# Kernel optimization log

Measured on AMD Instinct MI355X. Metric: run time of the kernel, lower is better.

## Reference

```python
import jax, jax.numpy as jnp
import numpy as np

HDIM = 1024
CDIM = 256
TEMPER = 10.0
IGNORE_OUT = 0.0
EPS = 1e-6


def setup_inputs() -> dict:
    key = jax.random.key(0)
    ks = jax.random.split(key, 6)
    B, T, D = 2, 128, 384
    x = jax.random.normal(ks[0], (B, T, D), jnp.float32)
    y = jax.random.normal(ks[1], (B, T, D), jnp.float32)
    # xavier-normal style init for the two linear layers
    W_enc = jax.random.normal(ks[2], (D, HDIM), jnp.float32) * np.sqrt(2.0 / (D + HDIM))
    b_enc = jnp.zeros((HDIM,), jnp.float32)
    W_dec = jax.random.normal(ks[3], (HDIM, D), jnp.float32) * np.sqrt(2.0 / (D + HDIM))
    b_dec = jnp.zeros((D,), jnp.float32)
    return {"x": x, "y": y, "W_enc": W_enc, "b_enc": b_enc, "W_dec": W_dec, "b_dec": b_dec}


def reference(x, y, W_enc, b_enc, W_dec, b_dec):
    B, T, D = x.shape
    n_iter = HDIM // CDIM
    pad = D - 1
    # shift_idx[s, j] = s + j : window of width D at offset s, s in [0, 2D-2]
    shift_idx = jnp.arange(2 * D - 1)[:, None] + jnp.arange(D)[None, :]

    seq_mask = (y == IGNORE_OUT)                       # (B,T,D) bool
    denom_seq = jnp.sum(~seq_mask).astype(x.dtype)
    qn = jnp.linalg.norm(y, axis=-1)                   # (B,T)

    mask_prev = None
    x_dis, losses = [], []
    for _ in range(n_iter):
        # --- _pad_for_shift: (B,T,2D-1,D) shifted windows of x ---
        kp = jnp.pad(x, ((0, 0), (0, 0), (pad, pad)))  # (B,T,3D-2)
        kpt = kp[..., shift_idx]                       # (B,T,2D-1,D)
        # --- _score (cos) + argmax over shifts ---
        kn = jnp.linalg.norm(kpt, axis=-1)             # (B,T,2D-1)
        sim = jnp.einsum('btsd,btd->bts', kpt, y) / (qn[..., None] * kn + EPS)
        sim = jnp.where(jnp.isnan(sim), 0.0, sim)
        theta = jnp.argmax(sim, axis=-1)               # (B,T) int
        x_opt = jnp.take_along_axis(kpt, theta[..., None, None], axis=-2)[..., 0, :]  # (B,T,D)
        # --- attention: elementwise cos-scaled score, temp softmax, detached ---
        dn = (jnp.linalg.norm(x_opt, axis=-1, keepdims=True)
              * jnp.linalg.norm(y, axis=-1, keepdims=True) + EPS)
        attn = jax.nn.softmax((x_opt * y / dn) / TEMPER, axis=-1)
        attn = jnp.where(jnp.isnan(attn), 0.0, attn)
        attn = jax.lax.stop_gradient(attn)
        x_attn = x_opt * attn
        # --- _reverse_pad_for_shift: window at offset 2D-2-theta ---
        kp2 = jnp.pad(x_attn, ((0, 0), (0, 0), (pad, pad)))
        rev_idx = (2 * D - 2 - theta)[..., None] + jnp.arange(D)  # (B,T,D)
        x_ele = jnp.take_along_axis(kp2, rev_idx, axis=-1)         # (B,T,D)
        # --- self_net: encoder -> top-k sparsify -> decoder_self ---
        h = x_ele @ W_enc + b_enc                      # (B,T,HDIM)
        if mask_prev is not None:
            h = jnp.where(mask_prev > 0, 1e-10, h)
        _, idx_top = jax.lax.top_k(h, CDIM)            # (B,T,CDIM)
        flat = idx_top.reshape(B * T, CDIM)
        mask_cur = jnp.zeros((B * T, HDIM), x.dtype).at[
            jnp.arange(B * T)[:, None], flat].set(1.0).reshape(B, T, HDIM)
        if mask_prev is None:
            mask_prev = mask_cur
        else:
            mask_prev = mask_prev + mask_cur - mask_prev * mask_cur
        h = h * mask_cur
        out = h @ W_dec + b_dec                        # (B,T,D)
        x_dis.append(out)
        # --- SeqLoss (masked MSE, mean-reduced by count of valid elems) ---
        err = jnp.where(seq_mask, 0.0, (out - x) ** 2) / denom_seq
        losses.append(jnp.sum(err))
    return jnp.stack(x_dis), jnp.stack(losses)
```

## Files before the change

### kernel.cpp

```cpp
#include <hip/hip_runtime.h>
#include <hip/hip_fp16.h>
#include <math.h>

#define DD 384
#define HD 1024
#define CD 256
#define NS 765
#define NITER 4
#define NROWS 256
#define TEMPER_F 10.0f
#define EPSF 1e-6f
#define CUTF 1e-10f

typedef unsigned long long u64;
typedef unsigned int u32;
typedef _Float16 hh2 __attribute__((ext_vector_type(2)));

__device__ __forceinline__ u32 flipf(float f) {
    u32 u = __float_as_uint(f);
    return u ^ ((u32)((int)u >> 31) | 0x80000000u);
}
__device__ __forceinline__ u32 packh2(float a, float b) {
    __half2 p = __floats2half2_rn(a, b);
    return __builtin_bit_cast(u32, p);
}
__device__ __forceinline__ float dot2(u32 a, u32 b, float c) {
#if __has_builtin(__builtin_amdgcn_fdot2)
    return __builtin_amdgcn_fdot2(__builtin_bit_cast(hh2, a),
                                  __builtin_bit_cast(hh2, b), c, false);
#else
    __half2 ah = __builtin_bit_cast(__half2, a);
    __half2 bh = __builtin_bit_cast(__half2, b);
    return fmaf(__half2float(ah.y), __half2float(bh.y),
           fmaf(__half2float(ah.x), __half2float(bh.x), c));
#endif
}

__global__ __launch_bounds__(256) void convert_kernel(
    const float* __restrict__ We, const float* __restrict__ Wd,
    uint4* __restrict__ wencp4, uint2* __restrict__ wd16)
{
    const int t = blockIdx.x * 256 + threadIdx.x;
    if (t < 192 * 256) {
        const int j2 = t >> 8, c4 = t & 255;
        float4 a = *(const float4*)&We[(2 * j2)     * HD + 4 * c4];
        float4 b = *(const float4*)&We[(2 * j2 + 1) * HD + 4 * c4];
        wencp4[j2 * 256 + c4] = make_uint4(packh2(a.x, b.x), packh2(a.y, b.y),
                                           packh2(a.z, b.z), packh2(a.w, b.w));
    }
    for (int i = t; i < (HD * DD) / 4; i += 65536) {
        float4 v = ((const float4*)Wd)[i];
        wd16[i] = make_uint2(packh2(v.x, v.y), packh2(v.z, v.w));
    }
}

__global__ __launch_bounds__(1024) void fused_kernel(
    const float* __restrict__ x, const float* __restrict__ y,
    const u32* __restrict__ wencp, const float* __restrict__ benc,
    const u32* __restrict__ wdec16, const float* __restrict__ bdec,
    float* __restrict__ out_xdis, float* __restrict__ lossp,
    int* __restrict__ ycnt)
{
    const int row  = blockIdx.x;
    const int tid  = threadIdx.x;
    const int lane = tid & 63;
    const int wid  = tid >> 6;

    __shared__ __align__(16) float xpad[1152];
    __shared__ __align__(16) float yr[DD];
    __shared__ u32   xep[192];
    __shared__ __align__(16) float part[4][HD];
    __shared__ __align__(16) u32   hist2[4096];
    __shared__ float spart[4 * 192 * 5];
    __shared__ __align__(16) uint2 dec2[HD];
    __shared__ __align__(16) float4 dpart[8][96];
    __shared__ float wred[16];
    __shared__ int   wredi[16];
    __shared__ float wredn[16];
    __shared__ int   wbase16[16];
    __shared__ float s_sc[4];
    __shared__ int   s_theta;
    __shared__ u32   s_b[3];
    __shared__ int   sbinB[3], srankB[3], s_cc[3];
    __shared__ u32   cand[3][64];
    __shared__ int   wcls[128];
    __shared__ int   sbase[128];
    __shared__ int   cnt8[8];
    __shared__ float loss4[NITER];

    const float* xrow = x + row * DD;
    const float* yrow = y + row * DD;

    for (int i = tid; i < 1152; i += 1024)
        xpad[i] = (i >= DD - 1 && i < 2 * DD - 1) ? xrow[i - (DD - 1)] : 0.f;
    if (tid < DD) yr[tid] = yrow[tid];
    __syncthreads();

    if (tid < 768) {
        const int qid = tid / 192, t = tid - qid * 192;
        const int jb = 24 * qid;
        const float4* xp4 = (const float4*)xpad;
        const float4* yp4 = (const float4*)yr;
        float4 A = xp4[t + jb];
        float d0 = 0.f, d1 = 0.f, d2 = 0.f, d3 = 0.f, n0 = 0.f;
#pragma unroll 8
        for (int jc = 0; jc < 24; ++jc) {
            float4 B = xp4[t + jb + jc + 1];
            float4 Y = yp4[jb + jc];
            d0 += A.x * Y.x; d0 += A.y * Y.y; d0 += A.z * Y.z; d0 += A.w * Y.w;
            d1 += A.y * Y.x; d1 += A.z * Y.y; d1 += A.w * Y.z; d1 += B.x * Y.w;
            d2 += A.z * Y.x; d2 += A.w * Y.y; d2 += B.x * Y.z; d2 += B.y * Y.w;
            d3 += A.w * Y.x; d3 += B.x * Y.y; d3 += B.y * Y.z; d3 += B.z * Y.w;
            n0 += A.x * A.x; n0 += A.y * A.y; n0 += A.z * A.z; n0 += A.w * A.w;
            A = B;
        }
        float* sp = &spart[(qid * 192 + t) * 5];
        sp[0] = d0; sp[1] = d1; sp[2] = d2; sp[3] = d3; sp[4] = n0;
    } else {
        const int i = tid - 768;
        if (i < 192) {
            float y0 = yr[2 * i], y1 = yr[2 * i + 1];
            float p = y0 * y0 + y1 * y1;
            int   c = (y0 != 0.f) + (y1 != 0.f);
            for (int o = 32; o; o >>= 1) {
                p += __shfl_xor(p, o, 64);
                c += __shfl_xor(c, o, 64);
            }
            if (lane == 0) { wred[wid] = p; wredi[wid] = c; }
            cand[i >> 6][i & 63] = 0xFFFFFFFFu;
        } else {
            const int j = i - 192;
            if (j < 3) s_cc[j] = 0;
            else if (j < 11) cnt8[j - 3] = 0;
            else if (j < 15) loss4[j - 11] = 0.f;
        }
        for (int h = i; h < 4096; h += 256) hist2[h] = 0u;
    }
    __syncthreads();

    if (tid < 192) {
        const float qn = sqrtf(wred[12] + wred[13] + wred[14]);
        const int b = tid * 5;
        float d0 = spart[b]     + spart[b + 960]     + spart[b + 1920]     + spart[b + 2880];
        float d1 = spart[b + 1] + spart[b + 961]     + spart[b + 1921]     + spart[b + 2881];
        float d2 = spart[b + 2] + spart[b + 962]     + spart[b + 1922]     + spart[b + 2882];
        float d3 = spart[b + 3] + spart[b + 963]     + spart[b + 1923]     + spart[b + 2883];
        float n0 = spart[b + 4] + spart[b + 964]     + spart[b + 1924]     + spart[b + 2884];
        const float x0 = xpad[4 * tid],       x1 = xpad[4 * tid + 1], x2 = xpad[4 * tid + 2];
        const float e0 = xpad[4 * tid + 384], e1 = xpad[4 * tid + 385], e2 = xpad[4 * tid + 386];
        const float n1 = n0 - x0 * x0 + e0 * e0;
        const float n2 = n1 - x1 * x1 + e1 * e1;
        const float n3 = n2 - x2 * x2 + e2 * e2;
        const int s0 = 4 * tid;
        float sim0 = d0 / (qn * sqrtf(n0) + EPSF);
        float sim1 = d1 / (qn * sqrtf(n1) + EPSF);
        float sim2 = d2 / (qn * sqrtf(n2) + EPSF);
        float sim3 = d3 / (qn * sqrtf(n3) + EPSF);
        float bv = sim0; int bs = s0; float bn = n0;
        if (s0 + 1 < NS && sim1 > bv) { bv = sim1; bs = s0 + 1; bn = n1; }
        if (s0 + 2 < NS && sim2 > bv) { bv = sim2; bs = s0 + 2; bn = n2; }
        if (s0 + 3 < NS && sim3 > bv) { bv = sim3; bs = s0 + 3; bn = n3; }
        for (int o = 32; o; o >>= 1) {
            float v2 = __shfl_xor(bv, o, 64);
            int   i2 = __shfl_xor(bs, o, 64);
            float nn2 = __shfl_xor(bn, o, 64);
            if (v2 > bv || (v2 == bv && i2 < bs)) { bv = v2; bs = i2; bn = nn2; }
        }
        if (lane == 0) { wred[wid] = bv; wredi[wid] = bs; wredn[wid] = bn; }
        if (tid == 0) s_sc[0] = qn;
    }
    if (tid == 960) ycnt[row] = wredi[12] + wredi[13] + wredi[14];
    __syncthreads();

    if (tid == 0) {
        float v = wred[0]; int b = wredi[0]; float nn = wredn[0];
        for (int w = 1; w < 3; ++w)
            if (wred[w] > v || (wred[w] == v && wredi[w] < b)) {
                v = wred[w]; b = wredi[w]; nn = wredn[w];
            }
        s_theta = b;
        s_sc[1] = sqrtf(nn) * s_sc[0] + EPSF;
    }
    __syncthreads();
    const int theta = s_theta;
    const float dn = s_sc[1];

    if (tid < DD) {
        float xo = xpad[theta + tid];
        float ez = expf((xo * yr[tid] / dn) / TEMPER_F);
        float p = ez;
        for (int o = 32; o; o >>= 1) p += __shfl_xor(p, o, 64);
        if (lane == 0) wred[wid] = p;
    }
    __syncthreads();

    if (tid < 192) {
        const float S = wred[0] + wred[1] + wred[2] + wred[3] + wred[4] + wred[5];
        const int off = theta - (DD - 1);
        const int sj = 2 * tid - off;
        float a0 = 0.f, a1 = 0.f;
        if (sj >= 0 && sj < DD) {
            float xo = xpad[theta + sj];
            a0 = xo * (expf((xo * yr[sj] / dn) / TEMPER_F) / S);
        }
        if (sj + 1 >= 0 && sj + 1 < DD) {
            float xo = xpad[theta + sj + 1];
            a1 = xo * (expf((xo * yr[sj + 1] / dn) / TEMPER_F) / S);
        }
        xep[tid] = packh2(a0, a1);
    }
    __syncthreads();

    {
        const int ks = tid >> 8;
        const int c4 = tid & 255;
        const uint4* wq = (const uint4*)wencp + (size_t)(ks * 48) * 256 + c4;
        const u32* xb = xep + ks * 48;
        float4 acc = make_float4(0.f, 0.f, 0.f, 0.f);
#pragma unroll 8
        for (int j2 = 0; j2 < 48; ++j2) {
            u32 xv = xb[j2];
            uint4 w = wq[(size_t)j2 * 256];
            acc.x = dot2(xv, w.x, acc.x);
            acc.y = dot2(xv, w.y, acc.y);
            acc.z = dot2(xv, w.z, acc.z);
            acc.w = dot2(xv, w.w, acc.w);
        }
        *(float4*)&part[ks][4 * c4] = acc;
    }
    __syncthreads();

    const float oh = part[0][tid] + part[1][tid] + part[2][tid] + part[3][tid]
                   + benc[tid];
    const u32 okey = ~flipf(oh);
    atomicAdd(&hist2[okey >> 20], 1u);
    __syncthreads();

    {
        const int t4 = tid << 2;
        const u32 l0 = hist2[t4], l1 = hist2[t4 + 1], l2 = hist2[t4 + 2], l3 = hist2[t4 + 3];
        const int s = (int)(l0 + l1 + l2 + l3);
        int inc = s;
        for (int o = 1; o < 64; o <<= 1) {
            int u = __shfl_up(inc, o, 64);
            if (lane >= o) inc += u;
        }
        if (lane == 63) wredi[wid] = inc;
        __syncthreads();
        if (tid == 0) {
            int acc = 0;
            for (int w = 0; w < 16; ++w) { wbase16[w] = acc; acc += wredi[w]; }
        }
        __syncthreads();
        const int c0 = wbase16[wid] + inc - s;
        const int c1 = c0 + (int)l0, c2 = c1 + (int)l1, c3 = c2 + (int)l2;
        const int c4e = c3 + (int)l3;
#pragma unroll
        for (int i = 0; i < 3; ++i) {
            const int R = 255 + (i << 8);
            if (R >= c0 && R < c1)      { sbinB[i] = t4;     srankB[i] = R - c0; }
            else if (R >= c1 && R < c2) { sbinB[i] = t4 + 1; srankB[i] = R - c1; }
            else if (R >= c2 && R < c3) { sbinB[i] = t4 + 2; srankB[i] = R - c2; }
            else if (R >= c3 && R < c4e){ sbinB[i] = t4 + 3; srankB[i] = R - c3; }
        }
        __syncthreads();
        const int myb = (int)(okey >> 20);
#pragma unroll
        for (int i = 0; i < 3; ++i) {
            if (myb == sbinB[i]) {
                int slot = atomicAdd(&s_cc[i], 1);
                if (slot < 64) cand[i][slot] = okey;
            }
        }
        __syncthreads();
        if (wid < 3) {
            u32 v = cand[wid][lane];
            for (int k2 = 2; k2 <= 64; k2 <<= 1) {
                for (int j = k2 >> 1; j > 0; j >>= 1) {
                    u32 p = __shfl_xor(v, j, 64);
                    const bool takeMin = ((lane & j) == 0) == ((lane & k2) == 0);
                    v = takeMin ? (v < p ? v : p) : (v > p ? v : p);
                }
            }
            if (lane == srankB[wid]) s_b[wid] = v;
        }
        __syncthreads();
    }
    const u32 b1 = s_b[0], b2 = s_b[1], b3 = s_b[2];

    {
        const int myk = (okey <= b1) ? 0 : (okey <= b2) ? 1 : (okey <= b3) ? 2 : 3;
        const int cls = 2 * myk + ((oh > CUTF) ? 0 : 1);
        int myprefix = 0;
        const u64 ltmask = (1ull << lane) - 1;
#pragma unroll
        for (int c = 0; c < 8; ++c) {
            u64 m = __ballot(cls == c);
            if (cls == c) myprefix = __popcll(m & ltmask);
            if (lane == 0) {
                wcls[c * 16 + wid] = (int)__popcll(m);
                atomicAdd(&cnt8[c], (int)__popcll(m));
            }
        }
        __syncthreads();
        if (tid < 128) {
            int v = wcls[tid];
            int inc = v;
            for (int o = 1; o < 64; o <<= 1) {
                int t2 = __shfl_up(inc, o, 64);
                if (lane >= o) inc += t2;
            }
            sbase[tid] = inc - v;
        }
        __syncthreads();
        if (tid >= 64 && tid < 128) sbase[tid] += sbase[63] + wcls[63];
        __syncthreads();
        const int slot = sbase[cls * 16 + wid] + myprefix;
        dec2[slot] = make_uint2(__float_as_uint(oh), (u32)tid * 192u);
    }
    __syncthreads();

    {
        const int g8 = tid >> 7;
        const int k  = g8 >> 1;
        const int hf = g8 & 1;
        const int gg = tid & 127;
        const bool active = (gg < 96);
        int n = 0;
        if (active) n = (k == 0) ? CD : cnt8[2 * k];
        int r  = hf * 128;
        int r1 = n < r + 128 ? n : r + 128;
        if (r1 < r) r1 = r;
        float4 acc = make_float4(0.f, 0.f, 0.f, 0.f);
        const u32* wd = wdec16 + 2 * gg;
        const int base = k * CD;
        for (; r + 8 <= r1; r += 8) {
#pragma unroll
            for (int q = 0; q < 8; q += 2) {
                uint4 dv = *(const uint4*)&dec2[base + r + q];
                u32 vp = packh2(__uint_as_float(dv.x), __uint_as_float(dv.z));
                uint2 w0 = *(const uint2*)(wd + dv.y);
                uint2 w1 = *(const uint2*)(wd + dv.w);
                u32 p0 = (w0.x & 0xffffu) | (w1.x << 16);
                u32 p1 = (w0.x >> 16) | (w1.x & 0xffff0000u);
                u32 p2 = (w0.y & 0xffffu) | (w1.y << 16);
                u32 p3 = (w0.y >> 16) | (w1.y & 0xffff0000u);
                acc.x = dot2(vp, p0, acc.x);
                acc.y = dot2(vp, p1, acc.y);
                acc.z = dot2(vp, p2, acc.z);
                acc.w = dot2(vp, p3, acc.w);
            }
        }
        for (; r + 2 <= r1; r += 2) {
            uint4 dv = *(const uint4*)&dec2[base + r];
            u32 vp = packh2(__uint_as_float(dv.x), __uint_as_float(dv.z));
            uint2 w0 = *(const uint2*)(wd + dv.y);
            uint2 w1 = *(const uint2*)(wd + dv.w);
            u32 p0 = (w0.x & 0xffffu) | (w1.x << 16);
            u32 p1 = (w0.x >> 16) | (w1.x & 0xffff0000u);
            u32 p2 = (w0.y & 0xffffu) | (w1.y << 16);
            u32 p3 = (w0.y >> 16) | (w1.y & 0xffff0000u);
            acc.x = dot2(vp, p0, acc.x);
            acc.y = dot2(vp, p1, acc.y);
            acc.z = dot2(vp, p2, acc.z);
            acc.w = dot2(vp, p3, acc.w);
        }
        if (r < r1) {
            uint2 dv = dec2[base + r];
            float v0 = __uint_as_float(dv.x);
            uint2 w0 = *(const uint2*)(wd + dv.y);
            u32 vlo = packh2(v0, 0.f), vhi = packh2(0.f, v0);
            acc.x = dot2(vlo, w0.x, acc.x);
            acc.y = dot2(vhi, w0.x, acc.y);
            acc.z = dot2(vlo, w0.y, acc.z);
            acc.w = dot2(vhi, w0.y, acc.w);
        }
        if (active) dpart[g8][gg] = acc;
    }
    __syncthreads();

    {
        float l = 0.f;
        if (tid < 512) {
            const int k2 = tid >> 7;
            const int q  = tid & 127;
            if (q < 96) {
                float4 a = dpart[2 * k2][q];
                float4 b = dpart[2 * k2 + 1][q];
                float4 bb = *(const float4*)&bdec[4 * q];
                float4 o4;
                o4.x = a.x + b.x + bb.x;
                o4.y = a.y + b.y + bb.y;
                o4.z = a.z + b.z + bb.z;
                o4.w = a.w + b.w + bb.w;
                *(float4*)&out_xdis[((size_t)k2 * NROWS + row) * DD + 4 * q] = o4;
                float4 xv = *(const float4*)&xrow[4 * q];
                float4 yv = *(const float4*)&yr[4 * q];
                float ee;
                ee = o4.x - xv.x; if (yv.x != 0.f) l += ee * ee;
                ee = o4.y - xv.y; if (yv.y != 0.f) l += ee * ee;
                ee = o4.z - xv.z; if (yv.z != 0.f) l += ee * ee;
                ee = o4.w - xv.w; if (yv.w != 0.f) l += ee * ee;
            }
        }
        for (int o = 32; o; o >>= 1) l += __shfl_xor(l, o, 64);
        if (tid < 512 && lane == 0) atomicAdd(&loss4[tid >> 7], l);
    }
    __syncthreads();
    if (tid < NITER) lossp[row * NITER + tid] = loss4[tid];
}

__global__ __launch_bounds__(256) void finalize2(
    const float* __restrict__ lossp, const int* __restrict__ ycnt,
    float* __restrict__ losses)
{
    const int tid = threadIdx.x, lane = tid & 63, w = tid >> 6;
    __shared__ int ctot[4];
    int c = ycnt[tid];
    for (int o = 32; o; o >>= 1) c += __shfl_xor(c, o, 64);
    if (lane == 0) ctot[w] = c;
    __syncthreads();
    const int total = ctot[0] + ctot[1] + ctot[2] + ctot[3];
    float s = lossp[lane * NITER + w] + lossp[(lane + 64) * NITER + w]
            + lossp[(lane + 128) * NITER + w] + lossp[(lane + 192) * NITER + w];
    for (int o = 32; o; o >>= 1) s += __shfl_xor(s, o, 64);
    if (lane == 0) losses[w] = s / (float)total;
}

extern "C" void kernel_launch(void* const* d_in, const int* in_sizes, int n_in,
                              void* d_out, int out_size, void* d_ws, size_t ws_size,
                              hipStream_t stream) {
    const float* x    = (const float*)d_in[0];
    const float* y    = (const float*)d_in[1];
    const float* Wenc = (const float*)d_in[2];
    const float* benc = (const float*)d_in[3];
    const float* Wdec = (const float*)d_in[4];
    const float* bdec = (const float*)d_in[5];

    float* out  = (float*)d_out;
    float* loss = out + (out_size - NITER);

    float* lossp  = (float*)d_ws;
    int*   ycnt   = (int*)(lossp + NROWS * NITER);
    u32*   wencp  = (u32*)(ycnt + NROWS);
    u32*   wdec16 = wencp + 192 * HD;

    convert_kernel<<<256, 256, 0, stream>>>(Wenc, Wdec, (uint4*)wencp,
                                            (uint2*)wdec16);
    fused_kernel<<<NROWS, 1024, 0, stream>>>(x, y, wencp, benc, wdec16, bdec,
                                             out, lossp, ycnt);
    finalize2<<<1, 256, 0, stream>>>(lossp, ycnt, loss);
}
```

Baseline: 99.24 us.

## Prefetch encoder weights early and remove a serial argmax/scan barrier

Loads the first twelve uint4 slices of the encoder weight and the encoder bias into registers at kernel start, so their global latency overlaps the shift-scoring phase. The final argmax across waves is folded into the softmax stage, which removes one block-wide barrier. The single-thread 16-entry prefix sum becomes a wave shuffle scan, and the histogram read uses one vector load. Decoder bias and x loads for the loss are also issued before the decoder loop. The cost is 48 extra VGPRs per thread at a 1024-thread block size, which could raise register pressure or cause spills.

```diff
diff --git a/kernel.cpp b/kernel.cpp
--- a/kernel.cpp
+++ b/kernel.cpp
@@ -11,6 +11,7 @@
 #define TEMPER_F 10.0f
 #define EPSF 1e-6f
 #define CUTF 1e-10f
+#define NPRE 12
 
 typedef unsigned long long u64;
 typedef unsigned int u32;
@@ -76,8 +77,10 @@
     __shared__ __align__(16) float4 dpart[8][96];
     __shared__ float wred[16];
     __shared__ int   wredi[16];
-    __shared__ float wredn[16];
     __shared__ int   wbase16[16];
+    __shared__ float s_bv[3];
+    __shared__ int   s_bi[3];
+    __shared__ float s_bn[3];
     __shared__ float s_sc[4];
     __shared__ int   s_theta;
     __shared__ u32   s_b[3];
@@ -90,6 +93,14 @@
 
     const float* xrow = x + row * DD;
     const float* yrow = y + row * DD;
+
+    const int eks = tid >> 8;
+    const int ec4 = tid & 255;
+    const uint4* wq = (const uint4*)wencp + (size_t)(eks * 48) * 256 + ec4;
+    uint4 wpre[NPRE];
+#pragma unroll
+    for (int p = 0; p < NPRE; ++p) wpre[p] = wq[(size_t)p * 256];
+    const float bpre = benc[tid];
 
     for (int i = tid; i < 1152; i += 1024)
         xpad[i] = (i >= DD - 1 && i < 2 * DD - 1) ? xrow[i - (DD - 1)] : 0.f;
@@ -141,11 +152,11 @@
     if (tid < 192) {
         const float qn = sqrtf(wred[12] + wred[13] + wred[14]);
         const int b = tid * 5;
-        float d0 = spart[b]     + spart[b + 960]     + spart[b + 1920]     + spart[b + 2880];
-        float d1 = spart[b + 1] + spart[b + 961]     + spart[b + 1921]     + spart[b + 2881];
-        float d2 = spart[b + 2] + spart[b + 962]     + spart[b + 1922]     + spart[b + 2882];
-        float d3 = spart[b + 3] + spart[b + 963]     + spart[b + 1923]     + spart[b + 2883];
-        float n0 = spart[b + 4] + spart[b + 964]     + spart[b + 1924]     + spart[b + 2884];
+        float d0 = spart[b]     + spart[b + 960] + spart[b + 1920] + spart[b + 2880];
+        float d1 = spart[b + 1] + spart[b + 961] + spart[b + 1921] + spart[b + 2881];
+        float d2 = spart[b + 2] + spart[b + 962] + spart[b + 1922] + spart[b + 2882];
+        float d3 = spart[b + 3] + spart[b + 963] + spart[b + 1923] + spart[b + 2883];
+        float n0 = spart[b + 4] + spart[b + 964] + spart[b + 1924] + spart[b + 2884];
         const float x0 = xpad[4 * tid],       x1 = xpad[4 * tid + 1], x2 = xpad[4 * tid + 2];
         const float e0 = xpad[4 * tid + 384], e1 = xpad[4 * tid + 385], e2 = xpad[4 * tid + 386];
         const float n1 = n0 - x0 * x0 + e0 * e0;
@@ -166,35 +177,30 @@
             float nn2 = __shfl_xor(bn, o, 64);
             if (v2 > bv || (v2 == bv && i2 < bs)) { bv = v2; bs = i2; bn = nn2; }
         }
-        if (lane == 0) { wred[wid] = bv; wredi[wid] = bs; wredn[wid] = bn; }
-        if (tid == 0) s_sc[0] = qn;
+        if (lane == 0) { s_bv[wid] = bv; s_bi[wid] = bs; s_bn[wid] = bn; }
     }
     if (tid == 960) ycnt[row] = wredi[12] + wredi[13] + wredi[14];
     __syncthreads();
 
-    if (tid == 0) {
-        float v = wred[0]; int b = wredi[0]; float nn = wredn[0];
-        for (int w = 1; w < 3; ++w)
-            if (wred[w] > v || (wred[w] == v && wredi[w] < b)) {
-                v = wred[w]; b = wredi[w]; nn = wredn[w];
-            }
-        s_theta = b;
-        s_sc[1] = sqrtf(nn) * s_sc[0] + EPSF;
-    }
-    __syncthreads();
-    const int theta = s_theta;
-    const float dn = s_sc[1];
-
     if (tid < DD) {
-        float xo = xpad[theta + tid];
-        float ez = expf((xo * yr[tid] / dn) / TEMPER_F);
+        const float qn2 = sqrtf(wred[12] + wred[13] + wred[14]);
+        float v = s_bv[0]; int b = s_bi[0]; float nn = s_bn[0];
+        if (s_bv[1] > v || (s_bv[1] == v && s_bi[1] < b)) { v = s_bv[1]; b = s_bi[1]; nn = s_bn[1]; }
+        if (s_bv[2] > v || (s_bv[2] == v && s_bi[2] < b)) { v = s_bv[2]; b = s_bi[2]; nn = s_bn[2]; }
+        const int th = b;
+        const float dnl = sqrtf(nn) * qn2 + EPSF;
+        float xo = xpad[th + tid];
+        float ez = expf((xo * yr[tid] / dnl) / TEMPER_F);
         float p = ez;
         for (int o = 32; o; o >>= 1) p += __shfl_xor(p, o, 64);
         if (lane == 0) wred[wid] = p;
+        if (tid == 0) { s_theta = th; s_sc[1] = dnl; }
     }
     __syncthreads();
 
     if (tid < 192) {
+        const int theta = s_theta;
+        const float dn = s_sc[1];
         const float S = wred[0] + wred[1] + wred[2] + wred[3] + wred[4] + wred[5];
         const int off = theta - (DD - 1);
         const int sj = 2 * tid - off;
@@ -212,13 +218,18 @@
     __syncthreads();
 
     {
-        const int ks = tid >> 8;
-        const int c4 = tid & 255;
-        const uint4* wq = (const uint4*)wencp + (size_t)(ks * 48) * 256 + c4;
-        const u32* xb = xep + ks * 48;
+        const u32* xb = xep + eks * 48;
         float4 acc = make_float4(0.f, 0.f, 0.f, 0.f);
-#pragma unroll 8
-        for (int j2 = 0; j2 < 48; ++j2) {
+#pragma unroll
+        for (int p = 0; p < NPRE; ++p) {
+            u32 xv = xb[p];
+            acc.x = dot2(xv, wpre[p].x, acc.x);
+            acc.y = dot2(xv, wpre[p].y, acc.y);
+            acc.z = dot2(xv, wpre[p].z, acc.z);
+            acc.w = dot2(xv, wpre[p].w, acc.w);
+        }
+#pragma unroll 6
+        for (int j2 = NPRE; j2 < 48; ++j2) {
             u32 xv = xb[j2];
             uint4 w = wq[(size_t)j2 * 256];
             acc.x = dot2(xv, w.x, acc.x);
@@ -226,19 +237,20 @@
             acc.z = dot2(xv, w.z, acc.z);
             acc.w = dot2(xv, w.w, acc.w);
         }
-        *(float4*)&part[ks][4 * c4] = acc;
+        *(float4*)&part[eks][4 * ec4] = acc;
     }
     __syncthreads();
 
     const float oh = part[0][tid] + part[1][tid] + part[2][tid] + part[3][tid]
-                   + benc[tid];
+                   + bpre;
     const u32 okey = ~flipf(oh);
     atomicAdd(&hist2[okey >> 20], 1u);
     __syncthreads();
 
     {
         const int t4 = tid << 2;
-        const u32 l0 = hist2[t4], l1 = hist2[t4 + 1], l2 = hist2[t4 + 2], l3 = hist2[t4 + 3];
+        const uint4 h4 = *(const uint4*)&hist2[t4];
+        const u32 l0 = h4.x, l1 = h4.y, l2 = h4.z, l3 = h4.w;
         const int s = (int)(l0 + l1 + l2 + l3);
         int inc = s;
         for (int o = 1; o < 64; o <<= 1) {
@@ -247,9 +259,14 @@
         }
         if (lane == 63) wredi[wid] = inc;
         __syncthreads();
-        if (tid == 0) {
-            int acc = 0;
-            for (int w = 0; w < 16; ++w) { wbase16[w] = acc; acc += wredi[w]; }
+        if (tid < 64) {
+            int vv = (lane < 16) ? wredi[lane] : 0;
+            int pr = vv;
+            for (int o = 1; o < 16; o <<= 1) {
+                int u2 = __shfl_up(pr, o, 64);
+                if (lane >= o) pr += u2;
+            }
+            if (lane < 16) wbase16[lane] = pr - vv;
         }
         __syncthreads();
         const int c0 = wbase16[wid] + inc - s;
@@ -320,6 +337,15 @@
     }
     __syncthreads();
 
+    float4 bb_pre = make_float4(0.f, 0.f, 0.f, 0.f);
+    float4 xv_pre = make_float4(0.f, 0.f, 0.f, 0.f);
+    {
+        const int qp = tid & 127;
+        if (tid < 512 && qp < 96) {
+            bb_pre = *(const float4*)&bdec[4 * qp];
+            xv_pre = *(const float4*)&xrow[4 * qp];
+        }
+    }
     {
         const int g8 = tid >> 7;
         const int k  = g8 >> 1;
@@ -387,20 +413,18 @@
             if (q < 96) {
                 float4 a = dpart[2 * k2][q];
                 float4 b = dpart[2 * k2 + 1][q];
-                float4 bb = *(const float4*)&bdec[4 * q];
                 float4 o4;
-                o4.x = a.x + b.x + bb.x;
-                o4.y = a.y + b.y + bb.y;
-                o4.z = a.z + b.z + bb.z;
-                o4.w = a.w + b.w + bb.w;
+                o4.x = a.x + b.x + bb_pre.x;
+                o4.y = a.y + b.y + bb_pre.y;
+                o4.z = a.z + b.z + bb_pre.z;
+                o4.w = a.w + b.w + bb_pre.w;
                 *(float4*)&out_xdis[((size_t)k2 * NROWS + row) * DD + 4 * q] = o4;
-                float4 xv = *(const float4*)&xrow[4 * q];
                 float4 yv = *(const float4*)&yr[4 * q];
                 float ee;
-                ee = o4.x - xv.x; if (yv.x != 0.f) l += ee * ee;
-                ee = o4.y - xv.y; if (yv.y != 0.f) l += ee * ee;
-                ee = o4.z - xv.z; if (yv.z != 0.f) l += ee * ee;
-                ee = o4.w - xv.w; if (yv.w != 0.f) l += ee * ee;
+                ee = o4.x - xv_pre.x; if (yv.x != 0.f) l += ee * ee;
+                ee = o4.y - xv_pre.y; if (yv.y != 0.f) l += ee * ee;
+                ee = o4.z - xv_pre.z; if (yv.z != 0.f) l += ee * ee;
+                ee = o4.w - xv_pre.w; if (yv.w != 0.f) l += ee * ee;
             }
         }
         for (int o = 32; o; o >>= 1) l += __shfl_xor(l, o, 64);
```

Result: no change. 99.13 us (-0.1%).
